# Optimization experiments

Hardware: AMD Instinct MI355X
Metric: run time of the kernel (lower is better)

Reference implementation:

```python
import jax, jax.numpy as jnp
import numpy as np

HID = 768        # config.hidden_size
MM_HID = 1024    # config.mmodal_hidden_size
N_Q = 64         # config.num_queries
WIN = 512        # config.window_size
LN_EPS = 1e-5


def _window_starts(m, n, w):
    # mirrors split_tensor's start-index logic (static, computed in numpy)
    step = max(1, (m - w) // (n - 1))
    starts = []
    for i in range(n):
        s = i * step
        if s + w > m:
            s = m - w
        starts.append(s)
    return np.asarray(starts, dtype=np.int32)


def layernorm(x, g, b):
    mu = jnp.mean(x, axis=-1, keepdims=True)
    var = jnp.var(x, axis=-1, keepdims=True)
    return (x - mu) * jax.lax.rsqrt(var + LN_EPS) * g + b


def setup_inputs() -> dict:
    key = jax.random.key(0)
    ks = jax.random.split(key, 12)
    b, m, li = 4, 8192, 77
    s = lambda fan_in: 1.0 / np.sqrt(fan_in)
    inp = {
        'x_mmodal': jax.random.normal(ks[0], (b, m, MM_HID), jnp.float32),
        'inst_feats': jax.random.normal(ks[1], (b, li, HID), jnp.float32),
        'queries': jax.random.normal(ks[2], (1, N_Q, HID), jnp.float32),
        'W_proj': jax.random.normal(ks[3], (HID, HID), jnp.float32) * s(HID),
        'b_proj': jnp.zeros((HID,), jnp.float32),
        'W_kv_inst': jax.random.normal(ks[4], (HID, 2 * HID), jnp.float32) * s(HID),
        'b_kv_inst': jnp.zeros((2 * HID,), jnp.float32),
        'W_out_inst': jax.random.normal(ks[5], (HID, HID), jnp.float32) * s(HID),
        'b_out_inst': jnp.zeros((HID,), jnp.float32),
        'W_kv_mm': jax.random.normal(ks[6], (MM_HID, 2 * HID), jnp.float32) * s(MM_HID),
        'b_kv_mm': jnp.zeros((2 * HID,), jnp.float32),
        'W_out_mm': jax.random.normal(ks[7], (HID, HID), jnp.float32) * s(HID),
        'b_out_mm': jnp.zeros((HID,), jnp.float32),
        'ln_g': jnp.ones((HID,), jnp.float32),
        'ln_b': jnp.zeros((HID,), jnp.float32),
    }
    return inp


def reference(x_mmodal, inst_feats, queries, W_proj, b_proj, W_kv_inst,
              b_kv_inst, W_out_inst, b_out_inst, W_kv_mm, b_kv_mm,
              W_out_mm, b_out_mm, ln_g, ln_b):
    b = x_mmodal.shape[0]
    scale = 1.0 / jnp.sqrt(jnp.asarray(HID, x_mmodal.dtype))

    # ---- dense cross-attention over instruction features ----
    inst = inst_feats @ W_proj + b_proj                      # (b, li, d)
    k, v = jnp.split(inst @ W_kv_inst + b_kv_inst, 2, axis=-1)
    k = layernorm(k, ln_g, ln_b)
    v = layernorm(v, ln_g, ln_b)
    q = jnp.broadcast_to(queries, (b, N_Q, HID))
    attn = jnp.einsum('bnd,bmd->bnm', q, k) * scale
    attn = jax.nn.softmax(attn, axis=-1)
    q = jnp.einsum('bnm,bmd->bnd', attn, v)
    q = layernorm(q @ W_out_inst + b_out_inst, ln_g, ln_b)

    # ---- swin-style overlapping windowed cross-attention over mmodal ----
    k, v = jnp.split(x_mmodal @ W_kv_mm + b_kv_mm, 2, axis=-1)
    k = layernorm(k, ln_g, ln_b)
    v = layernorm(v, ln_g, ln_b)
    m = k.shape[1]
    starts = _window_starts(m, N_Q, WIN)                     # (n,)
    idx = jnp.asarray(starts[:, None] + np.arange(WIN))      # (n, w)
    kw = k[:, idx]                                           # (b, n, w, d)
    vw = v[:, idx]                                           # (b, n, w, d)
    a = jnp.einsum('bnd,bnwd->bnw', q, kw) * scale
    a = jax.nn.softmax(a, axis=-1)
    out = jnp.einsum('bnw,bnwd->bnd', a, vw)
    out = layernorm(out @ W_out_mm + b_out_mm, ln_g, ln_b)
    return out
```

## Files before the change

kernel.cpp:

```cpp
#include <hip/hip_runtime.h>

#define HIDDEN 768
#define NQ 64
#define WINSZ 512
#define MSEQ 8192
#define BATCH 4
#define LI 77
#define MMHID 1024
#define LN_EPS 1e-5f
#define SCALE_QK 0.03608439182435161f

typedef __attribute__((ext_vector_type(8))) short short8v;
typedef __attribute__((ext_vector_type(4))) float f32x4;
typedef __attribute__((ext_vector_type(8))) unsigned short u16x8;

#define AS1 __attribute__((address_space(1)))
#define AS3 __attribute__((address_space(3)))

__device__ inline unsigned short f2bf(float f) {
    unsigned u = __float_as_uint(f);
    u += 0x7fffu + ((u >> 16) & 1u);
    return (unsigned short)(u >> 16);
}
__device__ inline float bf2f(unsigned short h) {
    return __uint_as_float(((unsigned)h) << 16);
}

__device__ inline void block_reduce2_256(float& s1, float& s2, float* sm) {
    #pragma unroll
    for (int o = 32; o; o >>= 1) { s1 += __shfl_down(s1, o); s2 += __shfl_down(s2, o); }
    int lane = threadIdx.x & 63, w = threadIdx.x >> 6;
    __syncthreads();
    if (lane == 0) { sm[w] = s1; sm[4 + w] = s2; }
    __syncthreads();
    s1 = sm[0] + sm[1] + sm[2] + sm[3];
    s2 = sm[4] + sm[5] + sm[6] + sm[7];
}

__global__ __launch_bounds__(256) void cvt_kernel(const float* __restrict__ in,
                                                  unsigned short* __restrict__ out, int n8) {
    int i = blockIdx.x * 256 + threadIdx.x;
    if (i >= n8) return;
    const float4* p = (const float4*)(in + (size_t)i * 8);
    float4 a = p[0], b = p[1];
    u16x8 o;
    o[0] = f2bf(a.x); o[1] = f2bf(a.y); o[2] = f2bf(a.z); o[3] = f2bf(a.w);
    o[4] = f2bf(b.x); o[5] = f2bf(b.y); o[6] = f2bf(b.z); o[7] = f2bf(b.w);
    *(u16x8*)(out + (size_t)i * 8) = o;
}

__global__ __launch_bounds__(256) void cvt_q_kernel(const float* __restrict__ q2,
                                                    const float* __restrict__ g,
                                                    const float* __restrict__ bb,
                                                    unsigned short* __restrict__ q2bf,
                                                    float* __restrict__ qgsum) {
    int blk = blockIdx.x;
    int b = blk >> 7, r = blk & 127;
    int t = threadIdx.x;
    __shared__ float sm[8];
    unsigned short* orow = q2bf + (size_t)blk * HIDDEN;
    if (r >= 64) {
        orow[t] = 0; orow[t + 256] = 0; orow[t + 512] = 0;
        return;
    }
    const float* qrow = q2 + ((size_t)(b * 64 + r)) * HIDDEN;
    float y0 = qrow[t], y1 = qrow[t + 256], y2 = qrow[t + 512];
    float s = y0 + y1 + y2, s2 = y0 * y0 + y1 * y1 + y2 * y2;
    block_reduce2_256(s, s2, sm);
    float mu = s * (1.f / 768.f);
    float var = s2 * (1.f / 768.f) - mu * mu;
    float inv = rsqrtf(var + LN_EPS);
    float qw0 = (y0 - mu) * inv * g[t]       + bb[t];
    float qw1 = (y1 - mu) * inv * g[t + 256] + bb[t + 256];
    float qw2 = (y2 - mu) * inv * g[t + 512] + bb[t + 512];
    float v0 = qw0 * g[t]       * SCALE_QK;
    float v1 = qw1 * g[t + 256] * SCALE_QK;
    float v2 = qw2 * g[t + 512] * SCALE_QK;
    orow[t] = f2bf(v0); orow[t + 256] = f2bf(v1); orow[t + 512] = f2bf(v2);
    float qs = v0 + v1 + v2, dummy = 0.f;
    block_reduce2_256(qs, dummy, sm);
    if (t == 0) qgsum[b * 64 + r] = qs;
}

struct PrepJobs {
    const float* W[5];
    unsigned short* Wt[5];
    int D[5];
    int C[5];
    const float* inst_in;
    unsigned short* inst_out;
    int n8_valid;
    int n8_total;
};
__global__ __launch_bounds__(256) void prep_kernel(PrepJobs tw) {
    int z = blockIdx.z;
    if (z == 5) {
        int flat = blockIdx.y * gridDim.x + blockIdx.x;
        int i = flat * 256 + threadIdx.x;
        if (i >= tw.n8_total) return;
        u16x8 o = {};
        if (i < tw.n8_valid) {
            const float4* p = (const float4*)(tw.inst_in + (size_t)i * 8);
            float4 a = p[0], b = p[1];
            o[0] = f2bf(a.x); o[1] = f2bf(a.y); o[2] = f2bf(a.z); o[3] = f2bf(a.w);
            o[4] = f2bf(b.x); o[5] = f2bf(b.y); o[6] = f2bf(b.z); o[7] = f2bf(b.w);
        }
        *(u16x8*)(tw.inst_out + (size_t)i * 8) = o;
        return;
    }
    int C = tw.C[z], D = tw.D[z];
    int n0 = blockIdx.x * 32, k0 = blockIdx.y * 32;
    if (n0 >= C || k0 >= D) return;
    const float* W = tw.W[z];
    unsigned short* Wt = tw.Wt[z];
    __shared__ float tile[32][33];
    int tx = threadIdx.x & 31, ty = (threadIdx.x >> 5);
    #pragma unroll
    for (int i = 0; i < 32; i += 8)
        tile[ty + i][tx] = W[(size_t)(k0 + ty + i) * C + n0 + tx];
    __syncthreads();
    #pragma unroll
    for (int i = 0; i < 32; i += 8)
        Wt[(size_t)(n0 + ty + i) * D + k0 + tx] = f2bf(tile[tx][ty + i]);
}

#define GM 32768
#define GN 1536
#define GK 1024

__global__ __launch_bounds__(512, 2) void gemm_kv256_kernel(const unsigned short* __restrict__ A,
                                                            const unsigned short* __restrict__ Bt,
                                                            const float* __restrict__ bias,
                                                            unsigned short* __restrict__ C) {
    extern __shared__ char smem[];
    unsigned short* sA = (unsigned short*)smem;
    unsigned short* sB = (unsigned short*)(smem + 65536);

    int nwg = gridDim.x;
    int bid = blockIdx.x;
    int wg = bid;
    if ((nwg & 7) == 0) { int cpx = nwg >> 3; wg = (bid & 7) * cpx + (bid >> 3); }
    int bm = wg / (GN / 256), bn = wg % (GN / 256);
    int row0 = bm * 256, col0 = bn * 256;

    int tid = threadIdx.x;
    int lane = tid & 63, wid = tid >> 6;
    int wm = wid >> 2, wn = wid & 3;

    f32x4 acc[8][4] = {};

    int rS[4], cS[4];
    #pragma unroll
    for (int i = 0; i < 4; i++) {
        int ch = wid * 4 + i;
        int r = ch * 8 + (lane >> 3);
        rS[i] = r;
        cS[i] = ((lane & 7) ^ (r & 7)) << 3;
    }

    auto STAGE = [&](int k0, int pbuf) {
        unsigned short* dA = sA + pbuf * 16384;
        unsigned short* dB = sB + pbuf * 16384;
        #pragma unroll
        for (int i = 0; i < 4; i++) {
            int ch = wid * 4 + i;
            const unsigned short* ga = A + (size_t)(row0 + rS[i]) * GK + k0 + cS[i];
            __builtin_amdgcn_global_load_lds((const AS1 unsigned int*)ga,
                                             (AS3 unsigned int*)&dA[ch * 512], 16, 0, 0);
            const unsigned short* gb = Bt + (size_t)(col0 + rS[i]) * GK + k0 + cS[i];
            __builtin_amdgcn_global_load_lds((const AS1 unsigned int*)gb,
                                             (AS3 unsigned int*)&dB[ch * 512], 16, 0, 0);
        }
    };

    STAGE(0, 0);
    __syncthreads();

    for (int kt = 0; kt < GK / 64; kt++) {
        int cur = kt & 1;
        if (kt < GK / 64 - 1) STAGE((kt + 1) * 64, cur ^ 1);

        const char* lA = (const char*)(sA + cur * 16384);
        const char* lB = (const char*)(sB + cur * 16384);

        short8v bfr[4][2];
        #pragma unroll
        for (int n = 0; n < 4; n++)
            #pragma unroll
            for (int kk = 0; kk < 2; kk++) {
                int r = wn * 64 + n * 16 + (lane & 15);
                int ko = (kk * 32 + ((lane >> 4) << 3)) * 2;
                bfr[n][kk] = *(const short8v*)(lB + r * 128 + (ko ^ ((r & 7) << 4)));
            }
        #pragma unroll
        for (int p = 0; p < 4; p++) {
            short8v afr[2][2];
            #pragma unroll
            for (int mf = 0; mf < 2; mf++)
                #pragma unroll
                for (int kk = 0; kk < 2; kk++) {
                    int r = wm * 128 + (p * 2 + mf) * 16 + (lane & 15);
                    int ko = (kk * 32 + ((lane >> 4) << 3)) * 2;
                    afr[mf][kk] = *(const short8v*)(lA + r * 128 + (ko ^ ((r & 7) << 4)));
                }
            __builtin_amdgcn_s_setprio(1);
            #pragma unroll
            for (int mf = 0; mf < 2; mf++)
                #pragma unroll
                for (int n = 0; n < 4; n++)
                    #pragma unroll
                    for (int kk = 0; kk < 2; kk++)
                        acc[p * 2 + mf][n] = __builtin_amdgcn_mfma_f32_16x16x32_bf16(
                            afr[mf][kk], bfr[n][kk], acc[p * 2 + mf][n], 0, 0, 0);
            __builtin_amdgcn_s_setprio(0);
        }
        __syncthreads();
    }

    int crow = (lane >> 4) * 4;
    int ccol = lane & 15;
    #pragma unroll
    for (int m = 0; m < 8; m++) {
        #pragma unroll
        for (int n = 0; n < 4; n++) {
            int gc = col0 + wn * 64 + n * 16 + ccol;
            float bv = bias[gc];
            #pragma unroll
            for (int j = 0; j < 4; j++) {
                int gr = row0 + wm * 128 + m * 16 + crow + j;
                C[(size_t)gr * GN + gc] = f2bf(acc[m][n][j] + bv);
            }
        }
    }
}

__global__ __launch_bounds__(256) void gemm_kv128_kernel(const unsigned short* __restrict__ A,
                                                         const unsigned short* __restrict__ Bt,
                                                         const float* __restrict__ bias,
                                                         unsigned short* __restrict__ C) {
    __shared__ unsigned short sA[128 * 64];
    __shared__ unsigned short sB[128 * 64];

    int nwg = gridDim.x;
    int bid = blockIdx.x;
    int wg = bid;
    if ((nwg & 7) == 0) { int cpx = nwg >> 3; wg = (bid & 7) * cpx + (bid >> 3); }
    int bm = wg / (GN / 128), bn = wg % (GN / 128);
    int row0 = bm * 128, col0 = bn * 128;

    int tid = threadIdx.x;
    int lane = tid & 63, wid = tid >> 6;
    int wr = wid >> 1, wc = wid & 1;

    f32x4 acc[4][4] = {};

    int rS[4], cS[4];
    #pragma unroll
    for (int i = 0; i < 4; i++) {
        int ch = wid * 4 + i;
        int r = ch * 8 + (lane >> 3);
        rS[i] = r;
        cS[i] = ((lane & 7) ^ (r & 7)) << 3;
    }

    for (int k0 = 0; k0 < GK; k0 += 64) {
        #pragma unroll
        for (int i = 0; i < 4; i++) {
            int ch = wid * 4 + i;
            const unsigned short* ga = A + (size_t)(row0 + rS[i]) * GK + k0 + cS[i];
            __builtin_amdgcn_global_load_lds((const AS1 unsigned int*)ga,
                                             (AS3 unsigned int*)&sA[ch * 512], 16, 0, 0);
            const unsigned short* gb = Bt + (size_t)(col0 + rS[i]) * GK + k0 + cS[i];
            __builtin_amdgcn_global_load_lds((const AS1 unsigned int*)gb,
                                             (AS3 unsigned int*)&sB[ch * 512], 16, 0, 0);
        }
        __syncthreads();

        #pragma unroll
        for (int kk = 0; kk < 64; kk += 32) {
            int ko = (kk + ((lane >> 4) << 3)) * 2;
            short8v af[4], bf[4];
            #pragma unroll
            for (int m = 0; m < 4; m++) {
                int r = wr * 64 + m * 16 + (lane & 15);
                int addr = r * 128 + (ko ^ ((r & 7) << 4));
                af[m] = *(const short8v*)((const char*)sA + addr);
            }
            #pragma unroll
            for (int n = 0; n < 4; n++) {
                int r = wc * 64 + n * 16 + (lane & 15);
                int addr = r * 128 + (ko ^ ((r & 7) << 4));
                bf[n] = *(const short8v*)((const char*)sB + addr);
            }
            #pragma unroll
            for (int m = 0; m < 4; m++)
                #pragma unroll
                for (int n = 0; n < 4; n++)
                    acc[m][n] = __builtin_amdgcn_mfma_f32_16x16x32_bf16(af[m], bf[n], acc[m][n], 0, 0, 0);
        }
        __syncthreads();
    }

    int crow = (lane >> 4) * 4;
    int ccol = lane & 15;
    #pragma unroll
    for (int m = 0; m < 4; m++) {
        #pragma unroll
        for (int n = 0; n < 4; n++) {
            int gc = col0 + wc * 64 + n * 16 + ccol;
            float bv = bias[gc];
            #pragma unroll
            for (int j = 0; j < 4; j++) {
                int gr = row0 + wr * 64 + m * 16 + crow + j;
                C[(size_t)gr * GN + gc] = f2bf(acc[m][n][j] + bv);
            }
        }
    }
}

__global__ __launch_bounds__(256) void stats_kernel(const unsigned short* __restrict__ kv,
                                                    float2* __restrict__ stats) {
    int rh = blockIdx.x;
    const unsigned short* p = kv + (size_t)rh * 768;
    int t = threadIdx.x;
    float x0 = bf2f(p[t]), x1 = bf2f(p[t + 256]), x2 = bf2f(p[t + 512]);
    float s = x0 + x1 + x2, s2 = x0 * x0 + x1 * x1 + x2 * x2;
    __shared__ float sm[8];
    block_reduce2_256(s, s2, sm);
    if (t == 0) {
        float mu = s * (1.f / 768.f);
        float var = s2 * (1.f / 768.f) - mu * mu;
        float inv = rsqrtf(var + LN_EPS);
        stats[rh] = make_float2(mu * inv, inv);
    }
}

template <int TK, bool OUT_BF16>
__global__ __launch_bounds__(256) void gemm_tile_kernel(const unsigned short* __restrict__ A,
                                                        const unsigned short* __restrict__ Bt,
                                                        const float* __restrict__ bias,
                                                        void* __restrict__ Cout, int N) {
    __shared__ unsigned short sA[128 * 64];
    __shared__ unsigned short sB[128 * 64];

    int row0 = blockIdx.x * 128, col0 = blockIdx.y * 128;
    int tid = threadIdx.x;
    int lane = tid & 63, wid = tid >> 6;
    int wr = wid >> 1, wc = wid & 1;

    f32x4 acc[4][4] = {};

    int rS[4], cS[4];
    #pragma unroll
    for (int i = 0; i < 4; i++) {
        int ch = wid * 4 + i;
        int r = ch * 8 + (lane >> 3);
        rS[i] = r;
        cS[i] = ((lane & 7) ^ (r & 7)) << 3;
    }

    for (int k0 = 0; k0 < TK; k0 += 64) {
        #pragma unroll
        for (int i = 0; i < 4; i++) {
            int ch = wid * 4 + i;
            const unsigned short* ga = A + (size_t)(row0 + rS[i]) * TK + k0 + cS[i];
            __builtin_amdgcn_global_load_lds((const AS1 unsigned int*)ga,
                                             (AS3 unsigned int*)&sA[ch * 512], 16, 0, 0);
            const unsigned short* gb = Bt + (size_t)(col0 + rS[i]) * TK + k0 + cS[i];
            __builtin_amdgcn_global_load_lds((const AS1 unsigned int*)gb,
                                             (AS3 unsigned int*)&sB[ch * 512], 16, 0, 0);
        }
        __syncthreads();

        #pragma unroll
        for (int kk = 0; kk < 64; kk += 32) {
            int ko = (kk + ((lane >> 4) << 3)) * 2;
            short8v af[4], bf[4];
            #pragma unroll
            for (int m = 0; m < 4; m++) {
                int r = wr * 64 + m * 16 + (lane & 15);
                int addr = r * 128 + (ko ^ ((r & 7) << 4));
                af[m] = *(const short8v*)((const char*)sA + addr);
            }
            #pragma unroll
            for (int n = 0; n < 4; n++) {
                int r = wc * 64 + n * 16 + (lane & 15);
                int addr = r * 128 + (ko ^ ((r & 7) << 4));
                bf[n] = *(const short8v*)((const char*)sB + addr);
            }
            #pragma unroll
            for (int m = 0; m < 4; m++)
                #pragma unroll
                for (int n = 0; n < 4; n++)
                    acc[m][n] = __builtin_amdgcn_mfma_f32_16x16x32_bf16(af[m], bf[n], acc[m][n], 0, 0, 0);
        }
        __syncthreads();
    }

    int crow = (lane >> 4) * 4;
    int ccol = lane & 15;
    #pragma unroll
    for (int m = 0; m < 4; m++) {
        #pragma unroll
        for (int n = 0; n < 4; n++) {
            int gc = col0 + wc * 64 + n * 16 + ccol;
            float bv = bias[gc];
            #pragma unroll
            for (int j = 0; j < 4; j++) {
                int gr = row0 + wr * 64 + m * 16 + crow + j;
                float v = acc[m][n][j] + bv;
                if (OUT_BF16) ((unsigned short*)Cout)[(size_t)gr * N + gc] = f2bf(v);
                else          ((float*)Cout)[(size_t)gr * N + gc] = v;
            }
        }
    }
}

__global__ __launch_bounds__(256) void gemm_scores_kernel(const unsigned short* __restrict__ Aall,
                                                          const unsigned short* __restrict__ kv,
                                                          float* __restrict__ scores) {
    __shared__ unsigned short sA[128 * 64];
    __shared__ unsigned short sB[128 * 64];

    int b = blockIdx.y;
    int col0 = blockIdx.x * 128;
    const unsigned short* A = Aall + (size_t)b * 128 * HIDDEN;
    const unsigned short* Bt = kv + (size_t)b * MSEQ * 1536;

    int tid = threadIdx.x;
    int lane = tid & 63, wid = tid >> 6;
    int wr = wid >> 1, wc = wid & 1;

    f32x4 acc[4][4] = {};

    int rS[4], cS[4];
    #pragma unroll
    for (int i = 0; i < 4; i++) {
        int ch = wid * 4 + i;
        int r = ch * 8 + (lane >> 3);
        rS[i] = r;
        cS[i] = ((lane & 7) ^ (r & 7)) << 3;
    }

    for (int k0 = 0; k0 < HIDDEN; k0 += 64) {
        #pragma unroll
        for (int i = 0; i < 4; i++) {
            int ch = wid * 4 + i;
            const unsigned short* ga = A + (size_t)rS[i] * HIDDEN + k0 + cS[i];
            __builtin_amdgcn_global_load_lds((const AS1 unsigned int*)ga,
                                             (AS3 unsigned int*)&sA[ch * 512], 16, 0, 0);
            const unsigned short* gb = Bt + (size_t)(col0 + rS[i]) * 1536 + k0 + cS[i];
            __builtin_amdgcn_global_load_lds((const AS1 unsigned int*)gb,
                                             (AS3 unsigned int*)&sB[ch * 512], 16, 0, 0);
        }
        __syncthreads();

        #pragma unroll
        for (int kk = 0; kk < 64; kk += 32) {
            int ko = (kk + ((lane >> 4) << 3)) * 2;
            short8v af[4], bf[4];
            #pragma unroll
            for (int m = 0; m < 4; m++) {
                int r = wr * 64 + m * 16 + (lane & 15);
                int addr = r * 128 + (ko ^ ((r & 7) << 4));
                af[m] = *(const short8v*)((const char*)sA + addr);
            }
            #pragma unroll
            for (int n = 0; n < 4; n++) {
                int r = wc * 64 + n * 16 + (lane & 15);
                int addr = r * 128 + (ko ^ ((r & 7) << 4));
                bf[n] = *(const short8v*)((const char*)sB + addr);
            }
            #pragma unroll
            for (int m = 0; m < 4; m++)
                #pragma unroll
                for (int n = 0; n < 4; n++)
                    acc[m][n] = __builtin_amdgcn_mfma_f32_16x16x32_bf16(af[m], bf[n], acc[m][n], 0, 0, 0);
        }
        __syncthreads();
    }

    int crow = (lane >> 4) * 4;
    int ccol = lane & 15;
    #pragma unroll
    for (int m = 0; m < 4; m++) {
        #pragma unroll
        for (int n = 0; n < 4; n++) {
            int gc = col0 + wc * 64 + n * 16 + ccol;
            #pragma unroll
            for (int j = 0; j < 4; j++) {
                int gr = wr * 64 + m * 16 + crow + j;
                if (gr < 64)
                    scores[((size_t)(b * 64 + gr)) * MSEQ + gc] = acc[m][n][j];
            }
        }
    }
}

__global__ __launch_bounds__(512) void win_softmax_kernel(const float* __restrict__ scores,
                                                          const float2* __restrict__ stats,
                                                          const float* __restrict__ qgsum,
                                                          unsigned short* __restrict__ P_abs,
                                                          float* __restrict__ s2out) {
    int bidx = blockIdx.x;
    int b = bidx >> 6, n = bidx & 63;
    int step = (MSEQ - WINSZ) / (NQ - 1);
    int s = n * step;
    if (s + WINSZ > MSEQ) s = MSEQ - WINSZ;

    __shared__ float sm[8];
    int t = threadIdx.x, lane = t & 63, w = t >> 6;
    int r_abs = s + t;
    size_t rowidx = (size_t)b * MSEQ + r_abs;
    float2 stk = stats[rowidx * 2 + 0];
    float qg = qgsum[b * 64 + n];
    float a = stk.y * scores[((size_t)(b * 64 + n)) * MSEQ + r_abs] - qg * stk.x;

    float m = a;
    #pragma unroll
    for (int o = 32; o; o >>= 1) m = fmaxf(m, __shfl_down(m, o));
    if (lane == 0) sm[w] = m;
    __syncthreads();
    m = sm[0];
    #pragma unroll
    for (int i = 1; i < 8; i++) m = fmaxf(m, sm[i]);
    float e = expf(a - m);
    float ssum = e;
    #pragma unroll
    for (int o = 32; o; o >>= 1) ssum += __shfl_down(ssum, o);
    __syncthreads();
    if (lane == 0) sm[w] = ssum;
    __syncthreads();
    ssum = 0;
    #pragma unroll
    for (int i = 0; i < 8; i++) ssum += sm[i];
    float p = e / ssum;

    float2 stv = stats[rowidx * 2 + 1];
    float pt = p * stv.y;
    float s2p = p * stv.x;
    #pragma unroll
    for (int o = 32; o; o >>= 1) s2p += __shfl_down(s2p, o);
    __syncthreads();
    if (lane == 0) sm[w] = s2p;
    __syncthreads();
    if (t == 0) {
        float s2 = 0;
        #pragma unroll
        for (int i = 0; i < 8; i++) s2 += sm[i];
        s2out[b * 64 + n] = s2;
    }

    unsigned short* prow = P_abs + ((size_t)(b * 64 + n)) * MSEQ;
    for (int pos = t; pos < MSEQ; pos += 512)
        if (pos < s || pos >= s + WINSZ) prow[pos] = 0;
    prow[r_abs] = f2bf(pt);
}

__global__ __launch_bounds__(768) void pv_chunk_kernel(const unsigned short* __restrict__ P_abs,
                                                       const unsigned short* __restrict__ kv,
                                                       float* __restrict__ out_acc) {
    int b = blockIdx.y;
    int r0 = blockIdx.x * 64;
    int t = threadIdx.x;

    int n_lo = (r0 >= 512) ? ((r0 - 512) / 121 + 1) : 0;
    int n_hi = (r0 + 63) / 121;
    if (n_hi > 63) n_hi = 63;

    __shared__ float pw[5][64];
    if (t < 5 * 64) {
        int ni = t >> 6, r = t & 63;
        int n = n_lo + ni;
        float v = 0.f;
        if (n <= n_hi)
            v = bf2f(P_abs[((size_t)(b * 64 + n)) * MSEQ + r0 + r]);
        pw[ni][r] = v;
    }
    __syncthreads();

    const unsigned short* vbase = kv + ((size_t)(b * MSEQ + r0)) * 1536 + 768;
    float acc[5] = {};
    #pragma unroll 8
    for (int r = 0; r < 64; ++r) {
        float v = bf2f(vbase[(size_t)r * 1536 + t]);
        #pragma unroll
        for (int ni = 0; ni < 5; ni++) acc[ni] = fmaf(v, pw[ni][r], acc[ni]);
    }
    #pragma unroll
    for (int ni = 0; ni < 5; ni++) {
        int n = n_lo + ni;
        if (n <= n_hi)
            atomicAdd(&out_acc[((size_t)(b * 64 + n)) * HIDDEN + t], acc[ni]);
    }
}

__global__ __launch_bounds__(256) void out_affine_kernel(const float* __restrict__ o_acc,
                                                         const float* __restrict__ s2,
                                                         const float* __restrict__ g,
                                                         const float* __restrict__ bb,
                                                         unsigned short* __restrict__ a_bf) {
    int i = blockIdx.x * 256 + threadIdx.x;
    if (i >= BATCH * NQ * HIDDEN) return;
    int n = i / HIDDEN, d = i - n * HIDDEN;
    a_bf[i] = f2bf(g[d] * (o_acc[i] - s2[n]) + bb[d]);
}

__global__ __launch_bounds__(256) void ln_f32_rows(float* __restrict__ base,
                                                   const float* __restrict__ g,
                                                   const float* __restrict__ b) {
    int rh = blockIdx.x;
    float* p = base + (size_t)rh * 768;
    int t = threadIdx.x;
    float x0 = p[t], x1 = p[t + 256], x2 = p[t + 512];
    float s = x0 + x1 + x2, s2 = x0 * x0 + x1 * x1 + x2 * x2;
    __shared__ float sm[8];
    block_reduce2_256(s, s2, sm);
    float mu = s * (1.f / 768.f);
    float var = s2 * (1.f / 768.f) - mu * mu;
    float inv = rsqrtf(var + LN_EPS);
    p[t]       = (x0 - mu) * inv * g[t]       + b[t];
    p[t + 256] = (x1 - mu) * inv * g[t + 256] + b[t + 256];
    p[t + 512] = (x2 - mu) * inv * g[t + 512] + b[t + 512];
}

__global__ __launch_bounds__(256) void attn_inst_kernel(const float* __restrict__ queries,
                                                        const float* __restrict__ kv,
                                                        unsigned short* __restrict__ qatt) {
    int bidx = blockIdx.x;
    int b = bidx >> 6, n = bidx & 63;
    __shared__ float qs[HIDDEN];
    __shared__ float sc[LI], sc2[LI];
    int t = threadIdx.x, lane = t & 63, w = t >> 6;
    const float* q = queries + (size_t)n * HIDDEN;
    for (int d = t; d < HIDDEN; d += 256) qs[d] = q[d];
    __syncthreads();
    const float* kb = kv + (size_t)b * LI * 1536;
    for (int j = w; j < LI; j += 4) {
        const float* kr = kb + (size_t)j * 1536;
        float a = 0;
        #pragma unroll
        for (int i = 0; i < 12; i++) { int d = lane + i * 64; a = fmaf(kr[d], qs[d], a); }
        #pragma unroll
        for (int o = 32; o; o >>= 1) a += __shfl_down(a, o);
        if (lane == 0) sc[j] = a * SCALE_QK;
    }
    __syncthreads();
    float m = -1e30f;
    for (int j = 0; j < LI; j++) m = fmaxf(m, sc[j]);
    if (t < LI) sc2[t] = expf(sc[t] - m);
    __syncthreads();
    float s = 0;
    for (int j = 0; j < LI; j++) s += sc2[j];
    float inv = 1.f / s;
    float o0 = 0, o1 = 0, o2 = 0;
    for (int j = 0; j < LI; j++) {
        float p = sc2[j] * inv;
        const float* vr = kb + (size_t)j * 1536 + 768;
        o0 = fmaf(p, vr[t], o0);
        o1 = fmaf(p, vr[t + 256], o1);
        o2 = fmaf(p, vr[t + 512], o2);
    }
    unsigned short* orow = qatt + ((size_t)b * NQ + n) * HIDDEN;
    orow[t] = f2bf(o0); orow[t + 256] = f2bf(o1); orow[t + 512] = f2bf(o2);
}

extern "C" void kernel_launch(void* const* d_in, const int* in_sizes, int n_in,
                              void* d_out, int out_size, void* d_ws, size_t ws_size,
                              hipStream_t stream) {
    (void)in_sizes; (void)n_in; (void)out_size; (void)ws_size;
    const float* x_mm    = (const float*)d_in[0];
    const float* instf   = (const float*)d_in[1];
    const float* queries = (const float*)d_in[2];
    const float* W_proj  = (const float*)d_in[3];
    const float* b_proj  = (const float*)d_in[4];
    const float* W_kvi   = (const float*)d_in[5];
    const float* b_kvi   = (const float*)d_in[6];
    const float* W_oi    = (const float*)d_in[7];
    const float* b_oi    = (const float*)d_in[8];
    const float* W_kvm   = (const float*)d_in[9];
    const float* b_kvm   = (const float*)d_in[10];
    const float* W_om    = (const float*)d_in[11];
    const float* b_om    = (const float*)d_in[12];
    const float* ln_g    = (const float*)d_in[13];
    const float* ln_b    = (const float*)d_in[14];
    float* out = (float*)d_out;

    char* ws = (char*)d_ws;
    size_t off = 0;
    auto carve = [&](size_t bytes) -> char* {
        char* p = ws + off;
        off += (bytes + 255) & ~(size_t)255;
        return p;
    };
    unsigned short* x_bf   = (unsigned short*)carve((size_t)BATCH * MSEQ * MMHID * 2);
    unsigned short* wtm_bf = (unsigned short*)carve((size_t)2 * HIDDEN * MMHID * 2);
    unsigned short* kv_mm  = (unsigned short*)carve((size_t)BATCH * MSEQ * 2 * HIDDEN * 2);
    unsigned short* wp_bf  = (unsigned short*)carve((size_t)768 * 768 * 2);
    unsigned short* wkvi_bf= (unsigned short*)carve((size_t)1536 * 768 * 2);
    unsigned short* woi_bf = (unsigned short*)carve((size_t)768 * 768 * 2);
    unsigned short* wom_bf = (unsigned short*)carve((size_t)768 * 768 * 2);
    unsigned short* a1_bf  = (unsigned short*)carve((size_t)384 * 768 * 2);
    unsigned short* inst_bf= (unsigned short*)carve((size_t)384 * 768 * 2);
    float*          kv_inst= (float*)carve((size_t)384 * 1536 * 4);
    unsigned short* qatt_bf= (unsigned short*)carve((size_t)256 * 768 * 2);
    float*          q2     = (float*)carve((size_t)256 * 768 * 4);
    unsigned short* q2bf   = (unsigned short*)carve((size_t)BATCH * 128 * 768 * 2);
    float*          scores = (float*)carve((size_t)BATCH * 64 * MSEQ * 4);
    unsigned short* P_abs  = (unsigned short*)carve((size_t)BATCH * 64 * MSEQ * 2);
    float*          o_acc  = (float*)carve((size_t)BATCH * 64 * 768 * 4);
    unsigned short* a_bf   = (unsigned short*)carve((size_t)256 * 768 * 2);
    float2*         stats  = (float2*)carve((size_t)BATCH * MSEQ * 2 * sizeof(float2));
    float*          qgsum  = (float*)carve((size_t)256 * 4);
    float*          s2     = (float*)carve((size_t)256 * 4);

    PrepJobs tw;
    tw.W[0] = W_kvm;  tw.Wt[0] = wtm_bf;  tw.D[0] = 1024; tw.C[0] = 1536;
    tw.W[1] = W_proj; tw.Wt[1] = wp_bf;   tw.D[1] = 768;  tw.C[1] = 768;
    tw.W[2] = W_kvi;  tw.Wt[2] = wkvi_bf; tw.D[2] = 768;  tw.C[2] = 1536;
    tw.W[3] = W_oi;   tw.Wt[3] = woi_bf;  tw.D[3] = 768;  tw.C[3] = 768;
    tw.W[4] = W_om;   tw.Wt[4] = wom_bf;  tw.D[4] = 768;  tw.C[4] = 768;
    tw.inst_in = instf; tw.inst_out = a1_bf;
    tw.n8_valid = BATCH * LI * 768 / 8; tw.n8_total = 384 * 768 / 8;
    prep_kernel<<<dim3(48, 32, 6), 256, 0, stream>>>(tw);

    int n8 = BATCH * MSEQ * MMHID / 8;
    cvt_kernel<<<(n8 + 255) / 256, 256, 0, stream>>>(x_mm, x_bf, n8);
    hipError_t attr_ok = hipFuncSetAttribute((const void*)gemm_kv256_kernel,
                                             hipFuncAttributeMaxDynamicSharedMemorySize, 131072);
    if (attr_ok == hipSuccess) {
        gemm_kv256_kernel<<<(GM / 256) * (GN / 256), 512, 131072, stream>>>(x_bf, wtm_bf, b_kvm, kv_mm);
    } else {
        gemm_kv128_kernel<<<(GM / 128) * (GN / 128), 256, 0, stream>>>(x_bf, wtm_bf, b_kvm, kv_mm);
    }
    stats_kernel<<<BATCH * MSEQ * 2, 256, 0, stream>>>(kv_mm, stats);

    gemm_tile_kernel<768, true><<<dim3(3, 6), 256, 0, stream>>>(a1_bf, wp_bf, b_proj, inst_bf, 768);
    gemm_tile_kernel<768, false><<<dim3(3, 12), 256, 0, stream>>>(inst_bf, wkvi_bf, b_kvi, kv_inst, 1536);
    ln_f32_rows<<<BATCH * LI * 2, 256, 0, stream>>>(kv_inst, ln_g, ln_b);
    attn_inst_kernel<<<BATCH * NQ, 256, 0, stream>>>(queries, kv_inst, qatt_bf);
    gemm_tile_kernel<768, false><<<dim3(2, 6), 256, 0, stream>>>(qatt_bf, woi_bf, b_oi, q2, 768);

    hipMemsetAsync(o_acc, 0, (size_t)BATCH * 64 * 768 * 4, stream);
    cvt_q_kernel<<<BATCH * 128, 256, 0, stream>>>(q2, ln_g, ln_b, q2bf, qgsum);
    gemm_scores_kernel<<<dim3(MSEQ / 128, BATCH), 256, 0, stream>>>(q2bf, kv_mm, scores);
    win_softmax_kernel<<<BATCH * NQ, 512, 0, stream>>>(scores, stats, qgsum, P_abs, s2);
    pv_chunk_kernel<<<dim3(MSEQ / 64, BATCH), 768, 0, stream>>>(P_abs, kv_mm, o_acc);
    out_affine_kernel<<<(BATCH * NQ * HIDDEN + 255) / 256, 256, 0, stream>>>(o_acc, s2, ln_g, ln_b, a_bf);

    gemm_tile_kernel<768, false><<<dim3(2, 6), 256, 0, stream>>>(a_bf, wom_bf, b_om, out, 768);
    ln_f32_rows<<<BATCH * NQ, 256, 0, stream>>>(out, ln_g, ln_b);
}
```

Measured before the change: 320.3 us.

## Fuse x conversion into prep, fold inst LayerNorm into attention, drop memset

```diff
diff --git a/kernel.cpp b/kernel.cpp
--- a/kernel.cpp
+++ b/kernel.cpp
@@ -35,18 +35,6 @@
     __syncthreads();
     s1 = sm[0] + sm[1] + sm[2] + sm[3];
     s2 = sm[4] + sm[5] + sm[6] + sm[7];
-}
-
-__global__ __launch_bounds__(256) void cvt_kernel(const float* __restrict__ in,
-                                                  unsigned short* __restrict__ out, int n8) {
-    int i = blockIdx.x * 256 + threadIdx.x;
-    if (i >= n8) return;
-    const float4* p = (const float4*)(in + (size_t)i * 8);
-    float4 a = p[0], b = p[1];
-    u16x8 o;
-    o[0] = f2bf(a.x); o[1] = f2bf(a.y); o[2] = f2bf(a.z); o[3] = f2bf(a.w);
-    o[4] = f2bf(b.x); o[5] = f2bf(b.y); o[6] = f2bf(b.z); o[7] = f2bf(b.w);
-    *(u16x8*)(out + (size_t)i * 8) = o;
 }
 
 __global__ __launch_bounds__(256) void cvt_q_kernel(const float* __restrict__ q2,
@@ -91,9 +79,27 @@
     unsigned short* inst_out;
     int n8_valid;
     int n8_total;
+    const float* x_in;
+    unsigned short* x_out;
+    int n8x;
 };
 __global__ __launch_bounds__(256) void prep_kernel(PrepJobs tw) {
     int z = blockIdx.z;
+    if (z >= 6) {
+        int per_slice = (int)(gridDim.x * gridDim.y);
+        int flat = blockIdx.y * gridDim.x + blockIdx.x;
+        int i0 = ((z - 6) * per_slice + flat) * 256 + threadIdx.x;
+        int stride = 2 * per_slice * 256;
+        for (int i = i0; i < tw.n8x; i += stride) {
+            const float4* p = (const float4*)(tw.x_in + (size_t)i * 8);
+            float4 a = p[0], b = p[1];
+            u16x8 o;
+            o[0] = f2bf(a.x); o[1] = f2bf(a.y); o[2] = f2bf(a.z); o[3] = f2bf(a.w);
+            o[4] = f2bf(b.x); o[5] = f2bf(b.y); o[6] = f2bf(b.z); o[7] = f2bf(b.w);
+            *(u16x8*)(tw.x_out + (size_t)i * 8) = o;
+        }
+        return;
+    }
     if (z == 5) {
         int flat = blockIdx.y * gridDim.x + blockIdx.x;
         int i = flat * 256 + threadIdx.x;
@@ -501,7 +507,8 @@
                                                           const float2* __restrict__ stats,
                                                           const float* __restrict__ qgsum,
                                                           unsigned short* __restrict__ P_abs,
-                                                          float* __restrict__ s2out) {
+                                                          float* __restrict__ s2out,
+                                                          float* __restrict__ o_acc) {
     int bidx = blockIdx.x;
     int b = bidx >> 6, n = bidx & 63;
     int step = (MSEQ - WINSZ) / (NQ - 1);
@@ -510,6 +517,11 @@
 
     __shared__ float sm[8];
     int t = threadIdx.x, lane = t & 63, w = t >> 6;
+
+    float* oz = o_acc + ((size_t)(b * 64 + n)) * HIDDEN;
+    oz[t] = 0.f;
+    if (t < 256) oz[512 + t] = 0.f;
+
     int r_abs = s + t;
     size_t rowidx = (size_t)b * MSEQ + r_abs;
     float2 stk = stats[rowidx * 2 + 0];
@@ -626,24 +638,53 @@
 
 __global__ __launch_bounds__(256) void attn_inst_kernel(const float* __restrict__ queries,
                                                         const float* __restrict__ kv,
+                                                        const float* __restrict__ g,
+                                                        const float* __restrict__ bb,
                                                         unsigned short* __restrict__ qatt) {
     int bidx = blockIdx.x;
     int b = bidx >> 6, n = bidx & 63;
-    __shared__ float qs[HIDDEN];
+    __shared__ float qg[HIDDEN];
     __shared__ float sc[LI], sc2[LI];
+    __shared__ float2 stv[LI];
+    __shared__ float sm[8];
     int t = threadIdx.x, lane = t & 63, w = t >> 6;
     const float* q = queries + (size_t)n * HIDDEN;
-    for (int d = t; d < HIDDEN; d += 256) qs[d] = q[d];
-    __syncthreads();
+    float pgs = 0.f, pqb = 0.f;
+    for (int d = t; d < HIDDEN; d += 256) {
+        float qd = q[d], gg = g[d];
+        qg[d] = qd * gg;
+        pgs += qd * gg;
+        pqb += qd * bb[d];
+    }
+    block_reduce2_256(pgs, pqb, sm);
+    float qgs = pgs, qb = pqb;
+
     const float* kb = kv + (size_t)b * LI * 1536;
     for (int j = w; j < LI; j += 4) {
         const float* kr = kb + (size_t)j * 1536;
-        float a = 0;
-        #pragma unroll
-        for (int i = 0; i < 12; i++) { int d = lane + i * 64; a = fmaf(kr[d], qs[d], a); }
-        #pragma unroll
-        for (int o = 32; o; o >>= 1) a += __shfl_down(a, o);
-        if (lane == 0) sc[j] = a * SCALE_QK;
+        const float* vr = kr + 768;
+        float dotg = 0, sk = 0, s2k = 0, sv = 0, s2v = 0;
+        #pragma unroll
+        for (int i = 0; i < 12; i++) {
+            int d = lane + i * 64;
+            float kd = kr[d], vd = vr[d];
+            dotg = fmaf(qg[d], kd, dotg);
+            sk += kd; s2k = fmaf(kd, kd, s2k);
+            sv += vd; s2v = fmaf(vd, vd, s2v);
+        }
+        #pragma unroll
+        for (int o = 32; o; o >>= 1) {
+            dotg += __shfl_down(dotg, o); sk += __shfl_down(sk, o); s2k += __shfl_down(s2k, o);
+            sv += __shfl_down(sv, o); s2v += __shfl_down(s2v, o);
+        }
+        if (lane == 0) {
+            float muk = sk * (1.f / 768.f);
+            float invk = rsqrtf(s2k * (1.f / 768.f) - muk * muk + LN_EPS);
+            sc[j] = SCALE_QK * (invk * dotg - muk * invk * qgs + qb);
+            float muv = sv * (1.f / 768.f);
+            float invv = rsqrtf(s2v * (1.f / 768.f) - muv * muv + LN_EPS);
+            stv[j] = make_float2(muv * invv, invv);
+        }
     }
     __syncthreads();
     float m = -1e30f;
@@ -652,17 +693,21 @@
     __syncthreads();
     float s = 0;
     for (int j = 0; j < LI; j++) s += sc2[j];
-    float inv = 1.f / s;
-    float o0 = 0, o1 = 0, o2 = 0;
+    float invs = 1.f / s;
+    float o0 = 0, o1 = 0, o2 = 0, s2sum = 0;
     for (int j = 0; j < LI; j++) {
-        float p = sc2[j] * inv;
+        float p = sc2[j] * invs;
+        float pt = p * stv[j].y;
+        s2sum = fmaf(p, stv[j].x, s2sum);
         const float* vr = kb + (size_t)j * 1536 + 768;
-        o0 = fmaf(p, vr[t], o0);
-        o1 = fmaf(p, vr[t + 256], o1);
-        o2 = fmaf(p, vr[t + 512], o2);
+        o0 = fmaf(pt, vr[t], o0);
+        o1 = fmaf(pt, vr[t + 256], o1);
+        o2 = fmaf(pt, vr[t + 512], o2);
     }
     unsigned short* orow = qatt + ((size_t)b * NQ + n) * HIDDEN;
-    orow[t] = f2bf(o0); orow[t + 256] = f2bf(o1); orow[t + 512] = f2bf(o2);
+    orow[t]       = f2bf(g[t]       * (o0 - s2sum) + bb[t]);
+    orow[t + 256] = f2bf(g[t + 256] * (o1 - s2sum) + bb[t + 256]);
+    orow[t + 512] = f2bf(g[t + 512] * (o2 - s2sum) + bb[t + 512]);
 }
 
 extern "C" void kernel_launch(void* const* d_in, const int* in_sizes, int n_in,
@@ -722,10 +767,9 @@
     tw.W[4] = W_om;   tw.Wt[4] = wom_bf;  tw.D[4] = 768;  tw.C[4] = 768;
     tw.inst_in = instf; tw.inst_out = a1_bf;
     tw.n8_valid = BATCH * LI * 768 / 8; tw.n8_total = 384 * 768 / 8;
-    prep_kernel<<<dim3(48, 32, 6), 256, 0, stream>>>(tw);
-
-    int n8 = BATCH * MSEQ * MMHID / 8;
-    cvt_kernel<<<(n8 + 255) / 256, 256, 0, stream>>>(x_mm, x_bf, n8);
+    tw.x_in = x_mm; tw.x_out = x_bf; tw.n8x = BATCH * MSEQ * MMHID / 8;
+    prep_kernel<<<dim3(48, 32, 8), 256, 0, stream>>>(tw);
+
     hipError_t attr_ok = hipFuncSetAttribute((const void*)gemm_kv256_kernel,
                                              hipFuncAttributeMaxDynamicSharedMemorySize, 131072);
     if (attr_ok == hipSuccess) {
@@ -737,14 +781,12 @@
 
     gemm_tile_kernel<768, true><<<dim3(3, 6), 256, 0, stream>>>(a1_bf, wp_bf, b_proj, inst_bf, 768);
     gemm_tile_kernel<768, false><<<dim3(3, 12), 256, 0, stream>>>(inst_bf, wkvi_bf, b_kvi, kv_inst, 1536);
-    ln_f32_rows<<<BATCH * LI * 2, 256, 0, stream>>>(kv_inst, ln_g, ln_b);
-    attn_inst_kernel<<<BATCH * NQ, 256, 0, stream>>>(queries, kv_inst, qatt_bf);
+    attn_inst_kernel<<<BATCH * NQ, 256, 0, stream>>>(queries, kv_inst, ln_g, ln_b, qatt_bf);
     gemm_tile_kernel<768, false><<<dim3(2, 6), 256, 0, stream>>>(qatt_bf, woi_bf, b_oi, q2, 768);
 
-    hipMemsetAsync(o_acc, 0, (size_t)BATCH * 64 * 768 * 4, stream);
     cvt_q_kernel<<<BATCH * 128, 256, 0, stream>>>(q2, ln_g, ln_b, q2bf, qgsum);
     gemm_scores_kernel<<<dim3(MSEQ / 128, BATCH), 256, 0, stream>>>(q2bf, kv_mm, scores);
-    win_softmax_kernel<<<BATCH * NQ, 512, 0, stream>>>(scores, stats, qgsum, P_abs, s2);
+    win_softmax_kernel<<<BATCH * NQ, 512, 0, stream>>>(scores, stats, qgsum, P_abs, s2, o_acc);
     pv_chunk_kernel<<<dim3(MSEQ / 64, BATCH), 768, 0, stream>>>(P_abs, kv_mm, o_acc);
     out_affine_kernel<<<(BATCH * NQ * HIDDEN + 255) / 256, 256, 0, stream>>>(o_acc, s2, ln_g, ln_b, a_bf);
 
```

Result: no change. 321.2 us (+0.3%).
